# Kernel tuning notes

Hardware: AMD Instinct MI355X
Metric: run time of the kernel (lower is better)

Reference implementation:

```python
import jax, jax.numpy as jnp
import numpy as np

B, N, H, NH = 2, 2048, 1024, 16
DH = H // NH  # 64
SCALE = H ** (-0.5)  # NOTE: original scales by hidden_size**-0.5, not head_dim**-0.5


def setup_inputs() -> dict:
    key = jax.random.key(0)
    k1, k2 = jax.random.split(key)
    hidden_states = jax.random.normal(k1, (B, N, H), dtype=jnp.float32)
    attention_mask = jnp.ones((B, N), dtype=jnp.int32)
    W_qkv = jax.random.normal(k2, (3 * H, H), dtype=jnp.float32) * (H ** -0.5)
    return {"hidden_states": hidden_states, "attention_mask": attention_mask, "W_qkv": W_qkv}


def reference(hidden_states, attention_mask, W_qkv):
    b, n, _ = hidden_states.shape
    # qkv: [b, n, 3H] = x @ W^T  (torch Linear, bias=False)
    qkv = jnp.einsum('bnd,ed->bne', hidden_states, W_qkv)
    # 'b n (k h d) -> k b h n d'
    qkv = qkv.reshape(b, n, 3, NH, DH)
    q, k, v = jnp.moveaxis(qkv, 2, 0).transpose(0, 1, 3, 2, 4)  # each [b, h, n, d]
    scores = jnp.einsum('bhid,bhjd->bhij', q, k) * SCALE
    # mask-fill: attention_mask[:, None, :, None] == 0 -> masks query rows (faithful)
    mask = (attention_mask[:, None, :, None] == 0)
    scores = jnp.where(mask, jnp.asarray(-10000.0, scores.dtype), scores)
    attn = jax.nn.softmax(scores, axis=-1)
    out = jnp.einsum('bhij,bhjd->bhid', attn, v)
    # 'b h n d -> b n (h d)'
    return out.transpose(0, 2, 1, 3).reshape(b, n, NH * DH)
```

## Files before the change

### kernel.cpp

```cpp
#include <hip/hip_runtime.h>
#include <hip/hip_bf16.h>
#include <stdint.h>

#define B_ 2
#define N_ 2048
#define H_ 1024
#define NH_ 16
#define DH_ 64
#define E_ 3072
#define M_ 4096
#define K_ 1024
#define QSCALE2_ 0.0450842200277786f
#define THR2_    11.5415603f

typedef unsigned short ushort_t;
typedef short bf16x8 __attribute__((ext_vector_type(8)));
typedef float f32x4 __attribute__((ext_vector_type(4)));
typedef ushort_t ushort8 __attribute__((ext_vector_type(8)));
typedef ushort_t ushort4v __attribute__((ext_vector_type(4)));
typedef float float4v __attribute__((ext_vector_type(4)));
typedef uint32_t uint2v __attribute__((ext_vector_type(2)));

static __device__ __forceinline__ ushort_t f2bf(float f) {
  __hip_bfloat16 h = __float2bfloat16(f);
  ushort_t u;
  __builtin_memcpy(&u, &h, sizeof(u));
  return u;
}
static __device__ __forceinline__ uint32_t pk2bf(float lo, float hi) {
  return (uint32_t)f2bf(lo) | ((uint32_t)f2bf(hi) << 16);
}
static __device__ __forceinline__ float max3f(float a, float b, float c) {
  return fmaxf(fmaxf(a, b), c);
}

#define GLOAD_LDS16(g, l)                                                   \
  __builtin_amdgcn_global_load_lds(                                         \
      (const __attribute__((address_space(1))) void*)(g),                   \
      (__attribute__((address_space(3))) void*)(l), 16, 0, 0)

__global__ void convert_kernel(const float* __restrict__ X,
                               const float* __restrict__ W,
                               ushort_t* __restrict__ Xb,
                               ushort_t* __restrict__ Wb) {
  const int nx4 = (M_ * K_) / 4;
  int i = blockIdx.x * blockDim.x + threadIdx.x;
  if (i < nx4) {
    float4v v = ((const float4v*)X)[i];
    ushort4v o;
    o[0] = f2bf(v[0]); o[1] = f2bf(v[1]); o[2] = f2bf(v[2]); o[3] = f2bf(v[3]);
    ((ushort4v*)Xb)[i] = o;
  } else {
    int j = i - nx4;
    float4v v = ((const float4v*)W)[j];
    ushort4v o;
    o[0] = f2bf(v[0]); o[1] = f2bf(v[1]); o[2] = f2bf(v[2]); o[3] = f2bf(v[3]);
    ((ushort4v*)Wb)[j] = o;
  }
}

__global__ void gemm_qkv(const ushort_t* __restrict__ Xb,
                         const ushort_t* __restrict__ Wb,
                         ushort_t* __restrict__ Qw,
                         ushort_t* __restrict__ Kw,
                         ushort_t* __restrict__ VTw) {
  __shared__ ushort_t lds_a[128 * 64];
  __shared__ ushort_t lds_b[128 * 64];
  const int tid = threadIdx.x;
  const int lane = tid & 63;
  const int w = tid >> 6;
  const int g = lane >> 4;
  const int l15 = lane & 15;
  const int wid = blockIdx.x;
  const int logical = (wid & 7) * 96 + (wid >> 3);
  const int m0 = (logical / 24) * 128;
  const int e0 = (logical % 24) * 128;
  const int wr = w >> 1, wc = w & 1;

  f32x4 zero = {0.f, 0.f, 0.f, 0.f};
  f32x4 acc[4][4];
#pragma unroll
  for (int mi = 0; mi < 4; ++mi)
#pragma unroll
    for (int ni = 0; ni < 4; ++ni) acc[mi][ni] = zero;

  for (int kt = 0; kt < K_ / 64; ++kt) {
    const int k0 = kt * 64;
#pragma unroll
    for (int i = 0; i < 4; ++i) {
      int chunk = i * 4 + w;
      int c = chunk * 64 + lane;
      int row = c >> 3;
      int col = (c & 7) * 8;
      GLOAD_LDS16(Xb + (size_t)(m0 + row) * K_ + k0 + col, lds_a + chunk * 512);
      GLOAD_LDS16(Wb + (size_t)(e0 + row) * K_ + k0 + col, lds_b + chunk * 512);
    }
    __syncthreads();
#pragma unroll
    for (int ks = 0; ks < 2; ++ks) {
      bf16x8 af[4], bfr[4];
#pragma unroll
      for (int mi = 0; mi < 4; ++mi)
        af[mi] = *(const bf16x8*)(lds_a + (wr * 64 + mi * 16 + l15) * 64 + ks * 32 + g * 8);
#pragma unroll
      for (int ni = 0; ni < 4; ++ni)
        bfr[ni] = *(const bf16x8*)(lds_b + (wc * 64 + ni * 16 + l15) * 64 + ks * 32 + g * 8);
#pragma unroll
      for (int mi = 0; mi < 4; ++mi)
#pragma unroll
        for (int ni = 0; ni < 4; ++ni)
          acc[mi][ni] = __builtin_amdgcn_mfma_f32_16x16x32_bf16(af[mi], bfr[ni], acc[mi][ni], 0, 0, 0);
    }
    __syncthreads();
  }

  const int kidx = e0 >> 10;
  if (kidx == 2) {
#pragma unroll
    for (int ni = 0; ni < 4; ++ni) {
      int e = e0 + wc * 64 + ni * 16 + l15;
      int h = (e >> 6) & 15;
      int d = e & 63;
#pragma unroll
      for (int mi = 0; mi < 4; ++mi) {
        int m = m0 + wr * 64 + mi * 16 + g * 4;
        int b = m >> 11;
        int n = m & (N_ - 1);
        ushort4v pk;
#pragma unroll
        for (int j = 0; j < 4; ++j) pk[j] = f2bf(acc[mi][ni][j]);
        *(ushort4v*)(VTw + ((size_t)(b * NH_ + h) * DH_ + d) * N_ + n) = pk;
      }
    }
  } else {
    ushort_t* dst = (kidx == 0) ? Qw : Kw;
    const float sc = (kidx == 0) ? QSCALE2_ : 1.0f;
#pragma unroll
    for (int ni = 0; ni < 4; ++ni) {
      int e = e0 + wc * 64 + ni * 16 + l15;
      int h = (e >> 6) & 15;
      int d = e & 63;
#pragma unroll
      for (int mi = 0; mi < 4; ++mi) {
#pragma unroll
        for (int j = 0; j < 4; ++j) {
          int m = m0 + wr * 64 + mi * 16 + g * 4 + j;
          int b = m >> 11;
          int n = m & (N_ - 1);
          dst[(size_t)((b * NH_ + h) * N_ + n) * DH_ + d] = f2bf(acc[mi][ni][j] * sc);
        }
      }
    }
  }
}

__global__ __launch_bounds__(256)
void attn_kernel(const ushort_t* __restrict__ Qw,
                 const ushort_t* __restrict__ Kw,
                 const ushort_t* __restrict__ VTw,
                 const int* __restrict__ amask,
                 float* __restrict__ out) {
  __shared__ ushort_t smem[16384 + 9216];
  ushort_t* lds_p = smem + 16384;

  const int tid = threadIdx.x;
  const int lane = tid & 63;
  const int w = tid >> 6;
  const int g = lane >> 4;
  const int l15 = lane & 15;
  const int wid = blockIdx.x;
  const int logical = (wid & 7) * 64 + (wid >> 3);
  const int bh = logical >> 4;
  const int b = bh >> 4, h = bh & 15;
  const int q0 = (logical & 15) * 128;

  const size_t base_nd = (size_t)bh * N_ * DH_;
  const size_t base_dn = (size_t)bh * DH_ * N_;

  const bf16x8 qzero = {0, 0, 0, 0, 0, 0, 0, 0};
  bf16x8 qf[2][2];
#pragma unroll
  for (int qi = 0; qi < 2; ++qi) {
    int q = q0 + w * 32 + qi * 16 + l15;
    int mq = amask[b * N_ + q];
#pragma unroll
    for (int ks = 0; ks < 2; ++ks) {
      bf16x8 v = *(const bf16x8*)(Qw + base_nd + (size_t)q * DH_ + ks * 32 + g * 8);
      qf[qi][ks] = mq ? v : qzero;
    }
  }

  const int st_r = (lane >> 3);
  const int st_s = (lane & 7) ^ st_r;

  f32x4 zero = {0.f, 0.f, 0.f, 0.f};
  f32x4 oacc[2][4];
#pragma unroll
  for (int qi = 0; qi < 2; ++qi)
#pragma unroll
    for (int df = 0; df < 4; ++df) oacc[qi][df] = zero;
  float m_run[2] = {-3.0e38f, -3.0e38f};
  float l_run[2] = {0.0f, 0.0f};

  const int NT = N_ / 64;

  {
#pragma unroll
    for (int i = 0; i < 2; ++i) {
      int chunk = w * 2 + i;
      int r = chunk * 8 + st_r;
      GLOAD_LDS16(Kw + base_nd + (size_t)r * DH_ + st_s * 8, smem + chunk * 512);
      GLOAD_LDS16(VTw + base_dn + (size_t)r * N_ + st_s * 8, smem + 4096 + chunk * 512);
    }
  }
  __syncthreads();

  for (int it = 0; it < NT; ++it) {
    const int cur = it & 1;
    ushort_t* lk = smem + cur * 8192;
    ushort_t* lv = smem + 4096 + cur * 8192;

    if (it + 1 < NT) {
      const int kv0n = (it + 1) * 64;
      ushort_t* nk = smem + (cur ^ 1) * 8192;
      ushort_t* nv = nk + 4096;
#pragma unroll
      for (int i = 0; i < 2; ++i) {
        int chunk = w * 2 + i;
        int r = chunk * 8 + st_r;
        GLOAD_LDS16(Kw + base_nd + (size_t)(kv0n + r) * DH_ + st_s * 8, nk + chunk * 512);
        GLOAD_LDS16(VTw + base_dn + (size_t)r * N_ + kv0n + st_s * 8, nv + chunk * 512);
      }
    }

    f32x4 sacc[2][4];
#pragma unroll
    for (int qi = 0; qi < 2; ++qi)
#pragma unroll
      for (int kvf = 0; kvf < 4; ++kvf) sacc[qi][kvf] = zero;
    __builtin_amdgcn_s_setprio(1);
#pragma unroll
    for (int ks = 0; ks < 2; ++ks) {
#pragma unroll
      for (int kvf = 0; kvf < 4; ++kvf) {
        bf16x8 a = *(const bf16x8*)(lk + (kvf * 16 + l15) * 64 +
                                    (((ks * 4 + g) ^ (l15 & 7)) * 8));
        sacc[0][kvf] = __builtin_amdgcn_mfma_f32_16x16x32_bf16(a, qf[0][ks], sacc[0][kvf], 0, 0, 0);
        sacc[1][kvf] = __builtin_amdgcn_mfma_f32_16x16x32_bf16(a, qf[1][ks], sacc[1][kvf], 0, 0, 0);
      }
    }
    __builtin_amdgcn_s_setprio(0);

    ushort_t* pw = lds_p + w * (32 * 72);
#pragma unroll
    for (int qi = 0; qi < 2; ++qi) {
      float a0 = max3f(sacc[qi][0][0], sacc[qi][0][1], sacc[qi][0][2]);
      float a1 = max3f(sacc[qi][0][3], sacc[qi][1][0], sacc[qi][1][1]);
      float a2 = max3f(sacc[qi][1][2], sacc[qi][1][3], sacc[qi][2][0]);
      float a3 = max3f(sacc[qi][2][1], sacc[qi][2][2], sacc[qi][2][3]);
      float a4 = max3f(sacc[qi][3][0], sacc[qi][3][1], sacc[qi][3][2]);
      float tm = fmaxf(max3f(a0, a1, a2), max3f(a3, a4, sacc[qi][3][3]));
      tm = fmaxf(tm, __shfl_xor(tm, 16));
      tm = fmaxf(tm, __shfl_xor(tm, 32));

      if (__any(tm > m_run[qi] + THR2_)) {
        float m_new = fmaxf(m_run[qi], tm);
        float alpha = exp2f(m_run[qi] - m_new);
        l_run[qi] *= alpha;
#pragma unroll
        for (int df = 0; df < 4; ++df)
#pragma unroll
          for (int j = 0; j < 4; ++j) oacc[qi][df][j] *= alpha;
        m_run[qi] = m_new;
      }

      float p[16];
#pragma unroll
      for (int kvf = 0; kvf < 4; ++kvf)
#pragma unroll
        for (int j = 0; j < 4; ++j)
          p[kvf * 4 + j] = exp2f(sacc[qi][kvf][j] - m_run[qi]);
      float t0 = (p[0] + p[1]) + (p[2] + p[3]);
      float t1 = (p[4] + p[5]) + (p[6] + p[7]);
      float t2 = (p[8] + p[9]) + (p[10] + p[11]);
      float t3 = (p[12] + p[13]) + (p[14] + p[15]);
      float ps = (t0 + t1) + (t2 + t3);
      ps += __shfl_xor(ps, 16);
      ps += __shfl_xor(ps, 32);
      l_run[qi] += ps;

#pragma unroll
      for (int kvf = 0; kvf < 4; ++kvf) {
        uint2v pkv;
        pkv[0] = pk2bf(p[kvf * 4 + 0], p[kvf * 4 + 1]);
        pkv[1] = pk2bf(p[kvf * 4 + 2], p[kvf * 4 + 3]);
        *(uint2v*)(pw + (qi * 16 + l15) * 72 + kvf * 16 + g * 4) = pkv;
      }
    }

    __builtin_amdgcn_s_setprio(1);
#pragma unroll
    for (int ks = 0; ks < 2; ++ks) {
      bf16x8 pb0 = *(const bf16x8*)(pw + (0 * 16 + l15) * 72 + ks * 32 + g * 8);
      bf16x8 pb1 = *(const bf16x8*)(pw + (1 * 16 + l15) * 72 + ks * 32 + g * 8);
#pragma unroll
      for (int df = 0; df < 4; ++df) {
        bf16x8 a = *(const bf16x8*)(lv + (df * 16 + l15) * 64 +
                                    (((ks * 4 + g) ^ (l15 & 7)) * 8));
        oacc[0][df] = __builtin_amdgcn_mfma_f32_16x16x32_bf16(a, pb0, oacc[0][df], 0, 0, 0);
        oacc[1][df] = __builtin_amdgcn_mfma_f32_16x16x32_bf16(a, pb1, oacc[1][df], 0, 0, 0);
      }
    }
    __builtin_amdgcn_s_setprio(0);
    __syncthreads();
  }

  float inv[2] = {1.0f / l_run[0], 1.0f / l_run[1]};
  float* osm = (float*)smem;
#pragma unroll
  for (int qi = 0; qi < 2; ++qi)
#pragma unroll
    for (int df = 0; df < 4; ++df)
#pragma unroll
      for (int j = 0; j < 4; ++j)
        osm[(w * 32 + qi * 16 + l15) * 68 + df * 16 + g * 4 + j] = oacc[qi][df][j] * inv[qi];
  __syncthreads();
  int d0 = (tid & 3) * 16;
#pragma unroll
  for (int rr = 0; rr < 2; ++rr) {
    int ql = rr * 64 + (tid >> 2);
    float* dst = out + ((size_t)(b * N_ + q0 + ql)) * H_ + h * DH_ + d0;
#pragma unroll
    for (int jj = 0; jj < 4; ++jj) {
      float4v v;
#pragma unroll
      for (int k = 0; k < 4; ++k) v[k] = osm[ql * 68 + d0 + jj * 4 + k];
      *(float4v*)(dst + jj * 4) = v;
    }
  }
}

extern "C" void kernel_launch(void* const* d_in, const int* in_sizes, int n_in,
                              void* d_out, int out_size, void* d_ws, size_t ws_size,
                              hipStream_t stream) {
  const float* X = (const float*)d_in[0];
  const int* amask = (const int*)d_in[1];
  const float* Wq = (const float*)d_in[2];
  float* out = (float*)d_out;
  char* ws = (char*)d_ws;
  ushort_t* Xb  = (ushort_t*)(ws);
  ushort_t* Wb  = (ushort_t*)(ws + 8388608);
  ushort_t* Qw  = (ushort_t*)(ws + 14680064);
  ushort_t* Kw  = (ushort_t*)(ws + 23068672);
  ushort_t* VTw = (ushort_t*)(ws + 31457280);

  convert_kernel<<<7168, 256, 0, stream>>>(X, Wq, Xb, Wb);
  gemm_qkv<<<768, 256, 0, stream>>>(Xb, Wb, Qw, Kw, VTw);
  attn_kernel<<<512, 256, 0, stream>>>(Qw, Kw, VTw, amask, out);
}
```

Baseline: 195.5 us.

## Use 8 waves per attention block with 16 query rows each

The attention kernel moves from 4 waves handling 32 query rows each to 8 waves handling 16 rows each, launched with 512 threads per block. Each K/V tile is loaded by 8 waves, one chunk per wave. Per-wave register state (accumulators, running max and sum) is halved, which should raise occupancy and latency hiding. In exchange, every K/V fragment read from LDS now feeds only one MFMA instead of two, so LDS traffic per FLOP doubles and barriers span more waves.

```diff
diff --git a/kernel.cpp b/kernel.cpp
--- a/kernel.cpp
+++ b/kernel.cpp
@@ -154,7 +154,7 @@
   }
 }
 
-__global__ __launch_bounds__(256)
+__global__ __launch_bounds__(512)
 void attn_kernel(const ushort_t* __restrict__ Qw,
                  const ushort_t* __restrict__ Kw,
                  const ushort_t* __restrict__ VTw,
@@ -178,15 +178,14 @@
   const size_t base_dn = (size_t)bh * DH_ * N_;
 
   const bf16x8 qzero = {0, 0, 0, 0, 0, 0, 0, 0};
-  bf16x8 qf[2][2];
-#pragma unroll
-  for (int qi = 0; qi < 2; ++qi) {
-    int q = q0 + w * 32 + qi * 16 + l15;
+  bf16x8 qf[2];
+  {
+    int q = q0 + w * 16 + l15;
     int mq = amask[b * N_ + q];
 #pragma unroll
     for (int ks = 0; ks < 2; ++ks) {
       bf16x8 v = *(const bf16x8*)(Qw + base_nd + (size_t)q * DH_ + ks * 32 + g * 8);
-      qf[qi][ks] = mq ? v : qzero;
+      qf[ks] = mq ? v : qzero;
     }
   }
 
@@ -194,24 +193,18 @@
   const int st_s = (lane & 7) ^ st_r;
 
   f32x4 zero = {0.f, 0.f, 0.f, 0.f};
-  f32x4 oacc[2][4];
-#pragma unroll
-  for (int qi = 0; qi < 2; ++qi)
-#pragma unroll
-    for (int df = 0; df < 4; ++df) oacc[qi][df] = zero;
-  float m_run[2] = {-3.0e38f, -3.0e38f};
-  float l_run[2] = {0.0f, 0.0f};
+  f32x4 oacc[4];
+#pragma unroll
+  for (int df = 0; df < 4; ++df) oacc[df] = zero;
+  float m_run = -3.0e38f;
+  float l_run = 0.0f;
 
   const int NT = N_ / 64;
 
   {
-#pragma unroll
-    for (int i = 0; i < 2; ++i) {
-      int chunk = w * 2 + i;
-      int r = chunk * 8 + st_r;
-      GLOAD_LDS16(Kw + base_nd + (size_t)r * DH_ + st_s * 8, smem + chunk * 512);
-      GLOAD_LDS16(VTw + base_dn + (size_t)r * N_ + st_s * 8, smem + 4096 + chunk * 512);
-    }
+    int r = w * 8 + st_r;
+    GLOAD_LDS16(Kw + base_nd + (size_t)r * DH_ + st_s * 8, smem + w * 512);
+    GLOAD_LDS16(VTw + base_dn + (size_t)r * N_ + st_s * 8, smem + 4096 + w * 512);
   }
   __syncthreads();
 
@@ -224,20 +217,14 @@
       const int kv0n = (it + 1) * 64;
       ushort_t* nk = smem + (cur ^ 1) * 8192;
       ushort_t* nv = nk + 4096;
-#pragma unroll
-      for (int i = 0; i < 2; ++i) {
-        int chunk = w * 2 + i;
-        int r = chunk * 8 + st_r;
-        GLOAD_LDS16(Kw + base_nd + (size_t)(kv0n + r) * DH_ + st_s * 8, nk + chunk * 512);
-        GLOAD_LDS16(VTw + base_dn + (size_t)r * N_ + kv0n + st_s * 8, nv + chunk * 512);
-      }
-    }
-
-    f32x4 sacc[2][4];
-#pragma unroll
-    for (int qi = 0; qi < 2; ++qi)
-#pragma unroll
-      for (int kvf = 0; kvf < 4; ++kvf) sacc[qi][kvf] = zero;
+      int r = w * 8 + st_r;
+      GLOAD_LDS16(Kw + base_nd + (size_t)(kv0n + r) * DH_ + st_s * 8, nk + w * 512);
+      GLOAD_LDS16(VTw + base_dn + (size_t)r * N_ + kv0n + st_s * 8, nv + w * 512);
+    }
+
+    f32x4 sacc[4];
+#pragma unroll
+    for (int kvf = 0; kvf < 4; ++kvf) sacc[kvf] = zero;
     __builtin_amdgcn_s_setprio(1);
 #pragma unroll
     for (int ks = 0; ks < 2; ++ks) {
@@ -245,33 +232,31 @@
       for (int kvf = 0; kvf < 4; ++kvf) {
         bf16x8 a = *(const bf16x8*)(lk + (kvf * 16 + l15) * 64 +
                                     (((ks * 4 + g) ^ (l15 & 7)) * 8));
-        sacc[0][kvf] = __builtin_amdgcn_mfma_f32_16x16x32_bf16(a, qf[0][ks], sacc[0][kvf], 0, 0, 0);
-        sacc[1][kvf] = __builtin_amdgcn_mfma_f32_16x16x32_bf16(a, qf[1][ks], sacc[1][kvf], 0, 0, 0);
+        sacc[kvf] = __builtin_amdgcn_mfma_f32_16x16x32_bf16(a, qf[ks], sacc[kvf], 0, 0, 0);
       }
     }
     __builtin_amdgcn_s_setprio(0);
 
-    ushort_t* pw = lds_p + w * (32 * 72);
-#pragma unroll
-    for (int qi = 0; qi < 2; ++qi) {
-      float a0 = max3f(sacc[qi][0][0], sacc[qi][0][1], sacc[qi][0][2]);
-      float a1 = max3f(sacc[qi][0][3], sacc[qi][1][0], sacc[qi][1][1]);
-      float a2 = max3f(sacc[qi][1][2], sacc[qi][1][3], sacc[qi][2][0]);
-      float a3 = max3f(sacc[qi][2][1], sacc[qi][2][2], sacc[qi][2][3]);
-      float a4 = max3f(sacc[qi][3][0], sacc[qi][3][1], sacc[qi][3][2]);
-      float tm = fmaxf(max3f(a0, a1, a2), max3f(a3, a4, sacc[qi][3][3]));
+    ushort_t* pw = lds_p + w * (16 * 72);
+    {
+      float a0 = max3f(sacc[0][0], sacc[0][1], sacc[0][2]);
+      float a1 = max3f(sacc[0][3], sacc[1][0], sacc[1][1]);
+      float a2 = max3f(sacc[1][2], sacc[1][3], sacc[2][0]);
+      float a3 = max3f(sacc[2][1], sacc[2][2], sacc[2][3]);
+      float a4 = max3f(sacc[3][0], sacc[3][1], sacc[3][2]);
+      float tm = fmaxf(max3f(a0, a1, a2), max3f(a3, a4, sacc[3][3]));
       tm = fmaxf(tm, __shfl_xor(tm, 16));
       tm = fmaxf(tm, __shfl_xor(tm, 32));
 
-      if (__any(tm > m_run[qi] + THR2_)) {
-        float m_new = fmaxf(m_run[qi], tm);
-        float alpha = exp2f(m_run[qi] - m_new);
-        l_run[qi] *= alpha;
+      if (__any(tm > m_run + THR2_)) {
+        float m_new = fmaxf(m_run, tm);
+        float alpha = exp2f(m_run - m_new);
+        l_run *= alpha;
 #pragma unroll
         for (int df = 0; df < 4; ++df)
 #pragma unroll
-          for (int j = 0; j < 4; ++j) oacc[qi][df][j] *= alpha;
-        m_run[qi] = m_new;
+          for (int j = 0; j < 4; ++j) oacc[df][j] *= alpha;
+        m_run = m_new;
       }
 
       float p[16];
@@ -279,7 +264,7 @@
       for (int kvf = 0; kvf < 4; ++kvf)
 #pragma unroll
         for (int j = 0; j < 4; ++j)
-          p[kvf * 4 + j] = exp2f(sacc[qi][kvf][j] - m_run[qi]);
+          p[kvf * 4 + j] = exp2f(sacc[kvf][j] - m_run);
       float t0 = (p[0] + p[1]) + (p[2] + p[3]);
       float t1 = (p[4] + p[5]) + (p[6] + p[7]);
       float t2 = (p[8] + p[9]) + (p[10] + p[11]);
@@ -287,56 +272,49 @@
       float ps = (t0 + t1) + (t2 + t3);
       ps += __shfl_xor(ps, 16);
       ps += __shfl_xor(ps, 32);
-      l_run[qi] += ps;
+      l_run += ps;
 
 #pragma unroll
       for (int kvf = 0; kvf < 4; ++kvf) {
         uint2v pkv;
         pkv[0] = pk2bf(p[kvf * 4 + 0], p[kvf * 4 + 1]);
         pkv[1] = pk2bf(p[kvf * 4 + 2], p[kvf * 4 + 3]);
-        *(uint2v*)(pw + (qi * 16 + l15) * 72 + kvf * 16 + g * 4) = pkv;
+        *(uint2v*)(pw + l15 * 72 + kvf * 16 + g * 4) = pkv;
       }
     }
 
     __builtin_amdgcn_s_setprio(1);
 #pragma unroll
     for (int ks = 0; ks < 2; ++ks) {
-      bf16x8 pb0 = *(const bf16x8*)(pw + (0 * 16 + l15) * 72 + ks * 32 + g * 8);
-      bf16x8 pb1 = *(const bf16x8*)(pw + (1 * 16 + l15) * 72 + ks * 32 + g * 8);
+      bf16x8 pb = *(const bf16x8*)(pw + l15 * 72 + ks * 32 + g * 8);
 #pragma unroll
       for (int df = 0; df < 4; ++df) {
         bf16x8 a = *(const bf16x8*)(lv + (df * 16 + l15) * 64 +
                                     (((ks * 4 + g) ^ (l15 & 7)) * 8));
-        oacc[0][df] = __builtin_amdgcn_mfma_f32_16x16x32_bf16(a, pb0, oacc[0][df], 0, 0, 0);
-        oacc[1][df] = __builtin_amdgcn_mfma_f32_16x16x32_bf16(a, pb1, oacc[1][df], 0, 0, 0);
+        oacc[df] = __builtin_amdgcn_mfma_f32_16x16x32_bf16(a, pb, oacc[df], 0, 0, 0);
       }
     }
     __builtin_amdgcn_s_setprio(0);
     __syncthreads();
   }
 
-  float inv[2] = {1.0f / l_run[0], 1.0f / l_run[1]};
+  float inv = 1.0f / l_run;
   float* osm = (float*)smem;
 #pragma unroll
-  for (int qi = 0; qi < 2; ++qi)
-#pragma unroll
-    for (int df = 0; df < 4; ++df)
-#pragma unroll
-      for (int j = 0; j < 4; ++j)
-        osm[(w * 32 + qi * 16 + l15) * 68 + df * 16 + g * 4 + j] = oacc[qi][df][j] * inv[qi];
+  for (int df = 0; df < 4; ++df)
+#pragma unroll
+    for (int j = 0; j < 4; ++j)
+      osm[(w * 16 + l15) * 68 + df * 16 + g * 4 + j] = oacc[df][j] * inv;
   __syncthreads();
   int d0 = (tid & 3) * 16;
-#pragma unroll
-  for (int rr = 0; rr < 2; ++rr) {
-    int ql = rr * 64 + (tid >> 2);
-    float* dst = out + ((size_t)(b * N_ + q0 + ql)) * H_ + h * DH_ + d0;
-#pragma unroll
-    for (int jj = 0; jj < 4; ++jj) {
-      float4v v;
-#pragma unroll
-      for (int k = 0; k < 4; ++k) v[k] = osm[ql * 68 + d0 + jj * 4 + k];
-      *(float4v*)(dst + jj * 4) = v;
-    }
+  int ql = tid >> 2;
+  float* dst = out + ((size_t)(b * N_ + q0 + ql)) * H_ + h * DH_ + d0;
+#pragma unroll
+  for (int jj = 0; jj < 4; ++jj) {
+    float4v v;
+#pragma unroll
+    for (int k = 0; k < 4; ++k) v[k] = osm[ql * 68 + d0 + jj * 4 + k];
+    *(float4v*)(dst + jj * 4) = v;
   }
 }
 
@@ -356,5 +334,5 @@
 
   convert_kernel<<<7168, 256, 0, stream>>>(X, Wq, Xb, Wb);
   gemm_qkv<<<768, 256, 0, stream>>>(Xb, Wb, Qw, Kw, VTw);
-  attn_kernel<<<512, 256, 0, stream>>>(Qw, Kw, VTw, amask, out);
-}
+  attn_kernel<<<512, 512, 0, stream>>>(Qw, Kw, VTw, amask, out);
+}
```

Measured after the change: 181.6 us. 1.08x faster.
